# Optimization experiments

Measured on AMD Instinct MI355X. Metric: run time of the kernel, lower is better.

The kernel has to match this reference:

```python
import jax, jax.numpy as jnp
import numpy as np

N, C_IN, NCLASS, H, W = 4, 32, 2, 64, 64


def setup_inputs() -> dict:
    key = jax.random.key(0)
    k1, k2, k3, k4, k5, k6 = jax.random.split(key, 6)
    return {
        "feature_in": jax.random.normal(k1, (N, C_IN, H, W), dtype=jnp.float32),
        "out": jax.random.normal(k2, (N, NCLASS, H, W), dtype=jnp.float32),
        "w1": jax.random.normal(k3, (NCLASS, C_IN), dtype=jnp.float32) * 0.1,
        "b1": jax.random.normal(k4, (NCLASS,), dtype=jnp.float32) * 0.1,
        "w2": jax.random.normal(k5, (NCLASS, C_IN), dtype=jnp.float32) * 0.1,
        "b2": jax.random.normal(k6, (NCLASS,), dtype=jnp.float32) * 0.1,
    }


def reference(feature_in, out, w1, b1, w2, b2):
    # h_in, w_in == input H, W (ceil(H/1)); bilinear resize to the same size
    # with align_corners=True is an exact identity, so no resampling is needed.
    n, c, h, w = feature_in.shape
    hw = h * w
    out = jax.lax.stop_gradient(out)  # out.detach() in the original

    # 1x1 convs == per-pixel linear projections
    f1 = jnp.einsum('nchw,kc->nkhw', feature_in, w1) + b1[None, :, None, None]
    f2 = jnp.einsum('nchw,kc->nkhw', feature_in, w2) + b2[None, :, None, None]
    f1 = f1.reshape(n, -1, hw)          # n k (h w)
    f2 = f2.reshape(n, -1, hw)
    out_flat = out.reshape(n, -1, hw)   # n c (h w)

    scale = 1.0 / jnp.sqrt(jnp.float32(f1.shape[1]))
    corr_map = jnp.einsum('nkp,nkq->npq', f1, f2) * scale  # [n, hw, hw]
    corr_map = jax.nn.softmax(corr_map, axis=-1)

    o = jnp.einsum('ncp,npq->ncq', out_flat, corr_map)
    return o.reshape(n, -1, h, w)
```

## Files before the change

kernel.cpp:

```cpp
#include <hip/hip_runtime.h>

#define HW   4096
#define CIN  32
#define SCALE2 (0.70710678118654752f * 1.44269504088896340f)

__device__ __forceinline__ float exp2_raw(float x) {
#if __has_builtin(__builtin_amdgcn_exp2f)
    return __builtin_amdgcn_exp2f(x);
#else
    float r;
    asm("v_exp_f32 %0, %1" : "=v"(r) : "v"(x));
    return r;
#endif
}

__global__ __launch_bounds__(256) void proj_kernel(
        const float* __restrict__ feat,
        const float* __restrict__ w1, const float* __restrict__ b1,
        const float* __restrict__ w2, const float* __restrict__ b2,
        float2* __restrict__ f1v, float2* __restrict__ f2v) {
    __shared__ float4 red[4][64];
    int tid = threadIdx.x;
    int pl = tid & 63;
    int cq = tid >> 6;
    int b = blockIdx.x;
    int n = b >> 6;
    int p = ((b & 63) << 6) + pl;
    const float* fbase = feat + ((size_t)n * CIN + cq * 8) * HW + p;
    float a10 = 0.f, a11 = 0.f, a20 = 0.f, a21 = 0.f;
#pragma unroll
    for (int c = 0; c < 8; ++c) {
        float v = fbase[(size_t)c * HW];
        a10 += v * w1[cq * 8 + c];
        a11 += v * w1[32 + cq * 8 + c];
        a20 += v * w2[cq * 8 + c];
        a21 += v * w2[32 + cq * 8 + c];
    }
    red[cq][pl] = make_float4(a10, a11, a20, a21);
    __syncthreads();
    if (tid < 64) {
        float4 r0 = red[0][tid], r1 = red[1][tid], r2 = red[2][tid], r3 = red[3][tid];
        int idx = n * HW + ((b & 63) << 6) + tid;
        f1v[idx] = make_float2(r0.x + r1.x + r2.x + r3.x + b1[0],
                               r0.y + r1.y + r2.y + r3.y + b1[1]);
        f2v[idx] = make_float2(r0.z + r1.z + r2.z + r3.z + b2[0],
                               r0.w + r1.w + r2.w + r3.w + b2[1]);
    }
}

__global__ __launch_bounds__(256) void rowstats_kernel(
        const float2* __restrict__ f1v, const float2* __restrict__ f2v,
        const float* __restrict__ outv, float4* __restrict__ stats4) {
    __shared__ float pB[4][17];
    int tid = threadIdx.x;
    int lane = tid & 63;
    int wid = tid >> 6;
    int b = blockIdx.x;
    int n = b >> 8;
    int pg = (b & 255) << 4;
    int base = n * HW;

    int ub = __builtin_amdgcn_readfirstlane(base + pg);
    float f10[16], f11[16];
#pragma unroll
    for (int j = 0; j < 16; ++j) {
        float2 f1 = f1v[ub + j];
        f10[j] = f1.x * SCALE2;
        f11[j] = f1.y * SCALE2;
    }
    const float4* f2b = (const float4*)(f2v + base) + wid * 512 + lane;
    float v[16];
#pragma unroll
    for (int j = 0; j < 16; ++j) v[j] = 0.f;
    float4 cur = f2b[0];
#pragma unroll
    for (int s = 0; s < 8; ++s) {
        float4 nxt = f2b[((s + 1) & 7) * 64];
#pragma unroll
        for (int j = 0; j < 16; ++j) {
            float e0 = exp2_raw(f10[j] * cur.x + f11[j] * cur.y);
            float e1 = exp2_raw(f10[j] * cur.z + f11[j] * cur.w);
            v[j] += e0 + e1;
        }
        cur = nxt;
    }
    {
        bool up8 = lane & 8;
#pragma unroll
        for (int k = 0; k < 8; ++k) {
            float send = up8 ? v[k] : v[k + 8];
            float recv = __shfl_xor(send, 8);
            v[k] = (up8 ? v[k + 8] : v[k]) + recv;
        }
        bool up4 = lane & 4;
#pragma unroll
        for (int k = 0; k < 4; ++k) {
            float send = up4 ? v[k] : v[k + 4];
            float recv = __shfl_xor(send, 4);
            v[k] = (up4 ? v[k + 4] : v[k]) + recv;
        }
        bool up2 = lane & 2;
#pragma unroll
        for (int k = 0; k < 2; ++k) {
            float send = up2 ? v[k] : v[k + 2];
            float recv = __shfl_xor(send, 2);
            v[k] = (up2 ? v[k + 2] : v[k]) + recv;
        }
        bool up1 = lane & 1;
        {
            float send = up1 ? v[0] : v[1];
            float recv = __shfl_xor(send, 1);
            v[0] = (up1 ? v[1] : v[0]) + recv;
        }
        v[0] += __shfl_xor(v[0], 16);
        v[0] += __shfl_xor(v[0], 32);
    }
    if (lane < 16) pB[wid][lane] = v[0];
    __syncthreads();
    if (tid < 16) {
        float lt = pB[0][tid] + pB[1][tid] + pB[2][tid] + pB[3][tid];
        float inv = 1.0f / lt;
        int pp = pg + tid;
        float2 f1 = f1v[base + pp];
        float v0 = outv[(n * 2 + 0) * HW + pp];
        float v1 = outv[(n * 2 + 1) * HW + pp];
        stats4[base + pp] = make_float4(f1.x * SCALE2, f1.y * SCALE2, v0 * inv, v1 * inv);
    }
}

__global__ __launch_bounds__(256) void colout_kernel(
        const float2* __restrict__ f2v, const float4* __restrict__ stats4,
        float* __restrict__ o) {
    __shared__ float pC[4][33];
    int tid = threadIdx.x;
    int lane = tid & 63;
    int wid = tid >> 6;
    int b = blockIdx.x;
    int n = b >> 8;
    int qg = (b & 255) << 4;
    int base = n * HW;

    int ub = __builtin_amdgcn_readfirstlane(base + qg);
    float g0[16], g1[16];
#pragma unroll
    for (int j = 0; j < 16; ++j) {
        float2 f2 = f2v[ub + j];
        g0[j] = f2.x;
        g1[j] = f2.y;
    }
    const float4* stb = stats4 + base + wid * 1024 + lane;
    float v[32];
#pragma unroll
    for (int j = 0; j < 32; ++j) v[j] = 0.f;
    float4 cur = stb[0];
#pragma unroll
    for (int s = 0; s < 16; ++s) {
        float4 nxt = stb[((s + 1) & 15) * 64];
#pragma unroll
        for (int j = 0; j < 16; ++j) {
            float e = exp2_raw(g0[j] * cur.x + g1[j] * cur.y);
            v[j]      += cur.z * e;
            v[16 + j] += cur.w * e;
        }
        cur = nxt;
    }
    {
        bool up16 = lane & 16;
#pragma unroll
        for (int k = 0; k < 16; ++k) {
            float send = up16 ? v[k] : v[k + 16];
            float recv = __shfl_xor(send, 16);
            v[k] = (up16 ? v[k + 16] : v[k]) + recv;
        }
        bool up8 = lane & 8;
#pragma unroll
        for (int k = 0; k < 8; ++k) {
            float send = up8 ? v[k] : v[k + 8];
            float recv = __shfl_xor(send, 8);
            v[k] = (up8 ? v[k + 8] : v[k]) + recv;
        }
        bool up4 = lane & 4;
#pragma unroll
        for (int k = 0; k < 4; ++k) {
            float send = up4 ? v[k] : v[k + 4];
            float recv = __shfl_xor(send, 4);
            v[k] = (up4 ? v[k + 4] : v[k]) + recv;
        }
        bool up2 = lane & 2;
#pragma unroll
        for (int k = 0; k < 2; ++k) {
            float send = up2 ? v[k] : v[k + 2];
            float recv = __shfl_xor(send, 2);
            v[k] = (up2 ? v[k + 2] : v[k]) + recv;
        }
        bool up1 = lane & 1;
        {
            float send = up1 ? v[0] : v[1];
            float recv = __shfl_xor(send, 1);
            v[0] = (up1 ? v[1] : v[0]) + recv;
        }
        v[0] += __shfl_xor(v[0], 32);
    }
    if (lane < 32) pC[wid][lane] = v[0];
    __syncthreads();
    if (tid < 32) {
        float r = pC[0][tid] + pC[1][tid] + pC[2][tid] + pC[3][tid];
        int ch = tid >> 4, qq = tid & 15;
        o[(n * 2 + ch) * HW + qg + qq] = r;
    }
}

extern "C" void kernel_launch(void* const* d_in, const int* in_sizes, int n_in,
                              void* d_out, int out_size, void* d_ws, size_t ws_size,
                              hipStream_t stream) {
    const float* feat = (const float*)d_in[0];
    const float* outv = (const float*)d_in[1];
    const float* w1   = (const float*)d_in[2];
    const float* b1   = (const float*)d_in[3];
    const float* w2   = (const float*)d_in[4];
    const float* b2   = (const float*)d_in[5];
    float* o = (float*)d_out;

    float*  ws     = (float*)d_ws;
    float2* f1v    = (float2*)ws;
    float2* f2v    = (float2*)(ws + 32768);
    float4* stats4 = (float4*)(ws + 65536);

    proj_kernel<<<256, 256, 0, stream>>>(feat, w1, b1, w2, b2, f1v, f2v);
    rowstats_kernel<<<1024, 256, 0, stream>>>(f1v, f2v, outv, stats4);
    colout_kernel<<<1024, 256, 0, stream>>>(f2v, stats4, o);
}
```

Baseline: 34.44 us.

## Fuse projection into rowstats kernel, recomputing f2 per block in LDS

Merges the projection kernel into the row-statistics kernel, which removes one launch and the f1 workspace round trip. Each 1024-thread block recomputes the full f2 projection for its batch image into shared memory. Only one block per image publishes f2 to global memory for the column kernel. This trades redundant projection work (every block reads all 32 input channels for 4096 pixels) and larger blocks with 32KB of LDS for fewer launches and LDS-resident f2 reads in the exp loop.

```diff
diff --git a/kernel.cpp b/kernel.cpp
--- a/kernel.cpp
+++ b/kernel.cpp
@@ -14,77 +14,77 @@
 #endif
 }
 
-__global__ __launch_bounds__(256) void proj_kernel(
-        const float* __restrict__ feat,
+__global__ __launch_bounds__(1024, 4) void rowstats_fused(
+        const float* __restrict__ feat, const float* __restrict__ outv,
         const float* __restrict__ w1, const float* __restrict__ b1,
         const float* __restrict__ w2, const float* __restrict__ b2,
-        float2* __restrict__ f1v, float2* __restrict__ f2v) {
-    __shared__ float4 red[4][64];
+        float2* __restrict__ f2v, float4* __restrict__ stats4) {
+    __shared__ float4 sf2[2048];
+    __shared__ float2 sf1[64];
+    __shared__ float  partial[16][16];
+
     int tid = threadIdx.x;
-    int pl = tid & 63;
-    int cq = tid >> 6;
+    int lane = tid & 63;
+    int w = tid >> 6;
     int b = blockIdx.x;
     int n = b >> 6;
-    int p = ((b & 63) << 6) + pl;
-    const float* fbase = feat + ((size_t)n * CIN + cq * 8) * HW + p;
-    float a10 = 0.f, a11 = 0.f, a20 = 0.f, a21 = 0.f;
-#pragma unroll
-    for (int c = 0; c < 8; ++c) {
-        float v = fbase[(size_t)c * HW];
-        a10 += v * w1[cq * 8 + c];
-        a11 += v * w1[32 + cq * 8 + c];
-        a20 += v * w2[cq * 8 + c];
-        a21 += v * w2[32 + cq * 8 + c];
-    }
-    red[cq][pl] = make_float4(a10, a11, a20, a21);
+    int pg = (b & 63) << 6;
+    int base = n * HW;
+    const float* fb = feat + (size_t)n * CIN * HW;
+
+    {
+        float a0[4] = {0.f, 0.f, 0.f, 0.f};
+        float a1[4] = {0.f, 0.f, 0.f, 0.f};
+        for (int c = 0; c < CIN; ++c) {
+            float wa = w2[c], wb = w2[CIN + c];
+            const float* fc = fb + (size_t)c * HW + tid;
+#pragma unroll
+            for (int k = 0; k < 4; ++k) {
+                float v = fc[k << 10];
+                a0[k] += v * wa;
+                a1[k] += v * wb;
+            }
+        }
+        float2* sf2f = (float2*)sf2;
+        bool pub = (b & 63) == 0;
+#pragma unroll
+        for (int k = 0; k < 4; ++k) {
+            float2 val = make_float2(a0[k] + b2[0], a1[k] + b2[1]);
+            sf2f[(k << 10) + tid] = val;
+            if (pub) f2v[base + (k << 10) + tid] = val;
+        }
+    }
+    if (tid < 128) {
+        int p = pg + (tid & 63);
+        int ch = tid >> 6;
+        float s = 0.f;
+        for (int c = 0; c < CIN; ++c) s += fb[(size_t)c * HW + p] * w1[ch * CIN + c];
+        ((float*)&sf1[tid & 63])[ch] = (s + b1[ch]) * SCALE2;
+    }
     __syncthreads();
-    if (tid < 64) {
-        float4 r0 = red[0][tid], r1 = red[1][tid], r2 = red[2][tid], r3 = red[3][tid];
-        int idx = n * HW + ((b & 63) << 6) + tid;
-        f1v[idx] = make_float2(r0.x + r1.x + r2.x + r3.x + b1[0],
-                               r0.y + r1.y + r2.y + r3.y + b1[1]);
-        f2v[idx] = make_float2(r0.z + r1.z + r2.z + r3.z + b2[0],
-                               r0.w + r1.w + r2.w + r3.w + b2[1]);
-    }
-}
-
-__global__ __launch_bounds__(256) void rowstats_kernel(
-        const float2* __restrict__ f1v, const float2* __restrict__ f2v,
-        const float* __restrict__ outv, float4* __restrict__ stats4) {
-    __shared__ float pB[4][17];
-    int tid = threadIdx.x;
-    int lane = tid & 63;
-    int wid = tid >> 6;
-    int b = blockIdx.x;
-    int n = b >> 8;
-    int pg = (b & 255) << 4;
-    int base = n * HW;
-
-    int ub = __builtin_amdgcn_readfirstlane(base + pg);
-    float f10[16], f11[16];
-#pragma unroll
-    for (int j = 0; j < 16; ++j) {
-        float2 f1 = f1v[ub + j];
-        f10[j] = f1.x * SCALE2;
-        f11[j] = f1.y * SCALE2;
-    }
-    const float4* f2b = (const float4*)(f2v + base) + wid * 512 + lane;
-    float v[16];
-#pragma unroll
-    for (int j = 0; j < 16; ++j) v[j] = 0.f;
-    float4 cur = f2b[0];
-#pragma unroll
-    for (int s = 0; s < 8; ++s) {
-        float4 nxt = f2b[((s + 1) & 7) * 64];
+
+    {
+        int pgrp = (w >> 2) << 4;
+        float f10[16], f11[16];
 #pragma unroll
         for (int j = 0; j < 16; ++j) {
-            float e0 = exp2_raw(f10[j] * cur.x + f11[j] * cur.y);
-            float e1 = exp2_raw(f10[j] * cur.z + f11[j] * cur.w);
-            v[j] += e0 + e1;
-        }
-        cur = nxt;
-    }
-    {
+            float2 t = sf1[pgrp + j];
+            f10[j] = t.x; f11[j] = t.y;
+        }
+        const float4* sp = sf2 + ((w & 3) << 9) + lane;
+        float v[16];
+#pragma unroll
+        for (int j = 0; j < 16; ++j) v[j] = 0.f;
+#pragma unroll
+        for (int s = 0; s < 8; ++s) {
+            float4 ab = sp[s * 64];
+#pragma unroll
+            for (int j = 0; j < 16; ++j) {
+                float e0 = exp2_raw(f10[j] * ab.x + f11[j] * ab.y);
+                float e1 = exp2_raw(f10[j] * ab.z + f11[j] * ab.w);
+                v[j] += e0 + e1;
+            }
+        }
         bool up8 = lane & 8;
 #pragma unroll
         for (int k = 0; k < 8; ++k) {
@@ -114,17 +114,20 @@
         }
         v[0] += __shfl_xor(v[0], 16);
         v[0] += __shfl_xor(v[0], 32);
-    }
-    if (lane < 16) pB[wid][lane] = v[0];
+        if (lane < 16) partial[w][lane] = v[0];
+    }
     __syncthreads();
-    if (tid < 16) {
-        float lt = pB[0][tid] + pB[1][tid] + pB[2][tid] + pB[3][tid];
-        float inv = 1.0f / lt;
+    if (tid < 64) {
+        int g4 = (tid >> 4) << 2;
+        int j = tid & 15;
+        float l = partial[g4][j] + partial[g4 + 1][j]
+                + partial[g4 + 2][j] + partial[g4 + 3][j];
+        float inv = 1.0f / l;
+        float2 f1 = sf1[tid];
         int pp = pg + tid;
-        float2 f1 = f1v[base + pp];
         float v0 = outv[(n * 2 + 0) * HW + pp];
         float v1 = outv[(n * 2 + 1) * HW + pp];
-        stats4[base + pp] = make_float4(f1.x * SCALE2, f1.y * SCALE2, v0 * inv, v1 * inv);
+        stats4[base + pp] = make_float4(f1.x, f1.y, v0 * inv, v1 * inv);
     }
 }
 
@@ -222,11 +225,9 @@
     float* o = (float*)d_out;
 
     float*  ws     = (float*)d_ws;
-    float2* f1v    = (float2*)ws;
-    float2* f2v    = (float2*)(ws + 32768);
-    float4* stats4 = (float4*)(ws + 65536);
-
-    proj_kernel<<<256, 256, 0, stream>>>(feat, w1, b1, w2, b2, f1v, f2v);
-    rowstats_kernel<<<1024, 256, 0, stream>>>(f1v, f2v, outv, stats4);
+    float2* f2v    = (float2*)ws;
+    float4* stats4 = (float4*)(ws + 32768);
+
+    rowstats_fused<<<256, 1024, 0, stream>>>(feat, outv, w1, b1, w2, b2, f2v, stats4);
     colout_kernel<<<1024, 256, 0, stream>>>(f2v, stats4, o);
 }
```

Result: slower. 48.06 us (+39.6%).

## Fuse projection, row-stats and column-output into one kernel with atomic grid barriers

Applied to the files above, without the earlier changes.

Merges the three kernels into one persistent-style launch. Per-batch atomic counters act as grid-level barriers between the f2 projection, the row-normalisation pass and the column-output pass, with a memset to reset the counters first. Each block recomputes its own f1 and f2 slices into shared memory, so the f1 buffer is no longer written or read globally. This removes two kernel launch gaps, at the cost of spin-waiting. It also relies on all 1024 blocks being co-resident (4 per CU assumed), otherwise the spin-waits can deadlock.

```diff
diff --git a/kernel.cpp b/kernel.cpp
--- a/kernel.cpp
+++ b/kernel.cpp
@@ -14,44 +14,18 @@
 #endif
 }
 
-__global__ __launch_bounds__(256) void proj_kernel(
-        const float* __restrict__ feat,
+__global__ __launch_bounds__(256, 4) void corr_fused(
+        const float* __restrict__ feat, const float* __restrict__ outv,
         const float* __restrict__ w1, const float* __restrict__ b1,
         const float* __restrict__ w2, const float* __restrict__ b2,
-        float2* __restrict__ f1v, float2* __restrict__ f2v) {
-    __shared__ float4 red[4][64];
-    int tid = threadIdx.x;
-    int pl = tid & 63;
-    int cq = tid >> 6;
-    int b = blockIdx.x;
-    int n = b >> 6;
-    int p = ((b & 63) << 6) + pl;
-    const float* fbase = feat + ((size_t)n * CIN + cq * 8) * HW + p;
-    float a10 = 0.f, a11 = 0.f, a20 = 0.f, a21 = 0.f;
-#pragma unroll
-    for (int c = 0; c < 8; ++c) {
-        float v = fbase[(size_t)c * HW];
-        a10 += v * w1[cq * 8 + c];
-        a11 += v * w1[32 + cq * 8 + c];
-        a20 += v * w2[cq * 8 + c];
-        a21 += v * w2[32 + cq * 8 + c];
-    }
-    red[cq][pl] = make_float4(a10, a11, a20, a21);
-    __syncthreads();
-    if (tid < 64) {
-        float4 r0 = red[0][tid], r1 = red[1][tid], r2 = red[2][tid], r3 = red[3][tid];
-        int idx = n * HW + ((b & 63) << 6) + tid;
-        f1v[idx] = make_float2(r0.x + r1.x + r2.x + r3.x + b1[0],
-                               r0.y + r1.y + r2.y + r3.y + b1[1]);
-        f2v[idx] = make_float2(r0.z + r1.z + r2.z + r3.z + b2[0],
-                               r0.w + r1.w + r2.w + r3.w + b2[1]);
-    }
-}
-
-__global__ __launch_bounds__(256) void rowstats_kernel(
-        const float2* __restrict__ f1v, const float2* __restrict__ f2v,
-        const float* __restrict__ outv, float4* __restrict__ stats4) {
-    __shared__ float pB[4][17];
+        float2* __restrict__ f2v, float4* __restrict__ stats4,
+        int* __restrict__ ctr, float* __restrict__ o) {
+    __shared__ float2 redP[4][64];
+    __shared__ float2 sf1[16];
+    __shared__ float2 sg[16];
+    __shared__ float  pB[4][17];
+    __shared__ float  pC[4][33];
+
     int tid = threadIdx.x;
     int lane = tid & 63;
     int wid = tid >> 6;
@@ -60,31 +34,77 @@
     int pg = (b & 255) << 4;
     int base = n * HW;
 
-    int ub = __builtin_amdgcn_readfirstlane(base + pg);
-    float f10[16], f11[16];
-#pragma unroll
-    for (int j = 0; j < 16; ++j) {
-        float2 f1 = f1v[ub + j];
-        f10[j] = f1.x * SCALE2;
-        f11[j] = f1.y * SCALE2;
-    }
-    const float4* f2b = (const float4*)(f2v + base) + wid * 512 + lane;
-    float v[16];
-#pragma unroll
-    for (int j = 0; j < 16; ++j) v[j] = 0.f;
-    float4 cur = f2b[0];
-#pragma unroll
-    for (int s = 0; s < 8; ++s) {
-        float4 nxt = f2b[((s + 1) & 7) * 64];
-#pragma unroll
-        for (int j = 0; j < 16; ++j) {
-            float e0 = exp2_raw(f10[j] * cur.x + f11[j] * cur.y);
-            float e1 = exp2_raw(f10[j] * cur.z + f11[j] * cur.w);
-            v[j] += e0 + e1;
-        }
-        cur = nxt;
-    }
+    if (b < 256) {
+        int np = b >> 6;
+        int col = ((b & 63) << 6) + lane;
+        const float* fbase = feat + ((size_t)np * CIN + wid * 8) * HW + col;
+        float a0 = 0.f, a1 = 0.f;
+#pragma unroll
+        for (int c = 0; c < 8; ++c) {
+            float v = fbase[(size_t)c * HW];
+            a0 += v * w2[wid * 8 + c];
+            a1 += v * w2[32 + wid * 8 + c];
+        }
+        redP[wid][lane] = make_float2(a0, a1);
+        __syncthreads();
+        if (tid < 64) {
+            float2 r0 = redP[0][tid], r1 = redP[1][tid], r2 = redP[2][tid], r3 = redP[3][tid];
+            f2v[np * HW + ((b & 63) << 6) + tid] =
+                make_float2(r0.x + r1.x + r2.x + r3.x + b2[0],
+                            r0.y + r1.y + r2.y + r3.y + b2[1]);
+        }
+        __syncthreads();
+        if (tid == 0)
+            __hip_atomic_fetch_add(&ctr[np << 5], 1, __ATOMIC_RELEASE,
+                                   __HIP_MEMORY_SCOPE_AGENT);
+    }
+
+    if (tid < 32) {
+        int pl = tid & 15, ch = tid >> 4;
+        const float* fp = feat + (size_t)n * CIN * HW + pg + pl;
+        const float* wr = w1 + ch * CIN;
+        float s = 0.f;
+#pragma unroll 8
+        for (int c = 0; c < CIN; ++c) s += fp[(size_t)c * HW] * wr[c];
+        ((float*)&sf1[pl])[ch] = (s + b1[ch]) * SCALE2;
+    } else if (tid < 64) {
+        int ql = tid & 15, ch = (tid >> 4) & 1;
+        const float* fp = feat + (size_t)n * CIN * HW + pg + ql;
+        const float* wr = w2 + ch * CIN;
+        float s = 0.f;
+#pragma unroll 8
+        for (int c = 0; c < CIN; ++c) s += fp[(size_t)c * HW] * wr[c];
+        ((float*)&sg[ql])[ch] = s + b2[ch];
+    }
+
+    if (tid == 0) {
+        while (__hip_atomic_load(&ctr[n << 5], __ATOMIC_RELAXED,
+                                 __HIP_MEMORY_SCOPE_AGENT) < 64)
+            __builtin_amdgcn_s_sleep(16);
+    }
+    __syncthreads();
+    __builtin_amdgcn_fence(__ATOMIC_ACQUIRE, "agent");
+
     {
+        float f10[16], f11[16];
+#pragma unroll
+        for (int j = 0; j < 16; ++j) { float2 t = sf1[j]; f10[j] = t.x; f11[j] = t.y; }
+        const float4* f2b = (const float4*)(f2v + base) + wid * 512 + lane;
+        float v[16];
+#pragma unroll
+        for (int j = 0; j < 16; ++j) v[j] = 0.f;
+        float4 cur = f2b[0];
+#pragma unroll
+        for (int s = 0; s < 8; ++s) {
+            float4 nxt = f2b[((s + 1) & 7) * 64];
+#pragma unroll
+            for (int j = 0; j < 16; ++j) {
+                float e0 = exp2_raw(f10[j] * cur.x + f11[j] * cur.y);
+                float e1 = exp2_raw(f10[j] * cur.z + f11[j] * cur.w);
+                v[j] += e0 + e1;
+            }
+            cur = nxt;
+        }
         bool up8 = lane & 8;
 #pragma unroll
         for (int k = 0; k < 8; ++k) {
@@ -114,57 +134,51 @@
         }
         v[0] += __shfl_xor(v[0], 16);
         v[0] += __shfl_xor(v[0], 32);
-    }
-    if (lane < 16) pB[wid][lane] = v[0];
+        if (lane < 16) pB[wid][lane] = v[0];
+    }
     __syncthreads();
     if (tid < 16) {
         float lt = pB[0][tid] + pB[1][tid] + pB[2][tid] + pB[3][tid];
         float inv = 1.0f / lt;
         int pp = pg + tid;
-        float2 f1 = f1v[base + pp];
+        float2 f1 = sf1[tid];
         float v0 = outv[(n * 2 + 0) * HW + pp];
         float v1 = outv[(n * 2 + 1) * HW + pp];
-        stats4[base + pp] = make_float4(f1.x * SCALE2, f1.y * SCALE2, v0 * inv, v1 * inv);
-    }
-}
-
-__global__ __launch_bounds__(256) void colout_kernel(
-        const float2* __restrict__ f2v, const float4* __restrict__ stats4,
-        float* __restrict__ o) {
-    __shared__ float pC[4][33];
-    int tid = threadIdx.x;
-    int lane = tid & 63;
-    int wid = tid >> 6;
-    int b = blockIdx.x;
-    int n = b >> 8;
-    int qg = (b & 255) << 4;
-    int base = n * HW;
-
-    int ub = __builtin_amdgcn_readfirstlane(base + qg);
-    float g0[16], g1[16];
-#pragma unroll
-    for (int j = 0; j < 16; ++j) {
-        float2 f2 = f2v[ub + j];
-        g0[j] = f2.x;
-        g1[j] = f2.y;
-    }
-    const float4* stb = stats4 + base + wid * 1024 + lane;
-    float v[32];
-#pragma unroll
-    for (int j = 0; j < 32; ++j) v[j] = 0.f;
-    float4 cur = stb[0];
-#pragma unroll
-    for (int s = 0; s < 16; ++s) {
-        float4 nxt = stb[((s + 1) & 15) * 64];
-#pragma unroll
-        for (int j = 0; j < 16; ++j) {
-            float e = exp2_raw(g0[j] * cur.x + g1[j] * cur.y);
-            v[j]      += cur.z * e;
-            v[16 + j] += cur.w * e;
-        }
-        cur = nxt;
-    }
+        stats4[base + pp] = make_float4(f1.x, f1.y, v0 * inv, v1 * inv);
+    }
+    __syncthreads();
+    if (tid == 0)
+        __hip_atomic_fetch_add(&ctr[1024 + (n << 5)], 1, __ATOMIC_RELEASE,
+                               __HIP_MEMORY_SCOPE_AGENT);
+
+    if (tid == 0) {
+        while (__hip_atomic_load(&ctr[1024 + (n << 5)], __ATOMIC_RELAXED,
+                                 __HIP_MEMORY_SCOPE_AGENT) < 256)
+            __builtin_amdgcn_s_sleep(32);
+    }
+    __syncthreads();
+    __builtin_amdgcn_fence(__ATOMIC_ACQUIRE, "agent");
+
     {
+        float g0[16], g1[16];
+#pragma unroll
+        for (int j = 0; j < 16; ++j) { float2 t = sg[j]; g0[j] = t.x; g1[j] = t.y; }
+        const float4* stb = stats4 + base + wid * 1024 + lane;
+        float v[32];
+#pragma unroll
+        for (int j = 0; j < 32; ++j) v[j] = 0.f;
+        float4 cur = stb[0];
+#pragma unroll
+        for (int s = 0; s < 16; ++s) {
+            float4 nxt = stb[((s + 1) & 15) * 64];
+#pragma unroll
+            for (int j = 0; j < 16; ++j) {
+                float e = exp2_raw(g0[j] * cur.x + g1[j] * cur.y);
+                v[j]      += cur.z * e;
+                v[16 + j] += cur.w * e;
+            }
+            cur = nxt;
+        }
         bool up16 = lane & 16;
 #pragma unroll
         for (int k = 0; k < 16; ++k) {
@@ -200,13 +214,13 @@
             v[0] = (up1 ? v[1] : v[0]) + recv;
         }
         v[0] += __shfl_xor(v[0], 32);
-    }
-    if (lane < 32) pC[wid][lane] = v[0];
+        if (lane < 32) pC[wid][lane] = v[0];
+    }
     __syncthreads();
     if (tid < 32) {
         float r = pC[0][tid] + pC[1][tid] + pC[2][tid] + pC[3][tid];
         int ch = tid >> 4, qq = tid & 15;
-        o[(n * 2 + ch) * HW + qg + qq] = r;
+        o[(n * 2 + ch) * HW + pg + qq] = r;
     }
 }
 
@@ -222,11 +236,12 @@
     float* o = (float*)d_out;
 
     float*  ws     = (float*)d_ws;
-    float2* f1v    = (float2*)ws;
-    float2* f2v    = (float2*)(ws + 32768);
-    float4* stats4 = (float4*)(ws + 65536);
-
-    proj_kernel<<<256, 256, 0, stream>>>(feat, w1, b1, w2, b2, f1v, f2v);
-    rowstats_kernel<<<1024, 256, 0, stream>>>(f1v, f2v, outv, stats4);
-    colout_kernel<<<1024, 256, 0, stream>>>(f2v, stats4, o);
+    float2* f2v    = (float2*)ws;
+    float4* stats4 = (float4*)(ws + 32768);
+    int*    ctr    = (int*)(ws + 32768 + 65536);
+
+    hipMemsetAsync(ctr, 0, 8192, stream);
+
+    corr_fused<<<1024, 256, 0, stream>>>(feat, outv, w1, b1, w2, b2,
+                                         f2v, stats4, ctr, o);
 }
```

After: 124.4 us. 261% more time.
